# Optimization experiments

Hardware: AMD Instinct MI355X
Metric: run time of the kernel (lower is better)

Reference implementation:

```python
import jax, jax.numpy as jnp
import numpy as np

E, T, H, I, K = 8, 8192, 1024, 4096, 2  # experts, tokens, hidden, intermediate, top_k


def setup_inputs() -> dict:
    key = jax.random.key(0)
    k1, k2, k3, k4 = jax.random.split(key, 4)
    return {
        "hidden_states": jax.random.normal(k1, (T, H), dtype=jnp.float32),
        "router_weight": jax.random.normal(k2, (E, H), dtype=jnp.float32) * 0.02,
        "gate_up_proj": jax.random.normal(k3, (E, 2 * I, H), dtype=jnp.float32) * 0.02,
        "down_proj": jax.random.normal(k4, (E, H, I), dtype=jnp.float32) * 0.02,
    }


def reference(hidden_states, router_weight, gate_up_proj, down_proj):
    x = hidden_states  # [T, H]
    # --- TopKRouter ---
    router_logits = x @ router_weight.T  # [T, E]
    routing_probs = jax.nn.softmax(router_logits.astype(jnp.float32), axis=-1)
    top_k_weights, top_k_indices = jax.lax.top_k(routing_probs, K)  # [T, K]
    top_k_weights = top_k_weights / jnp.sum(top_k_weights, axis=-1, keepdims=True)  # norm_topk_prob
    top_k_weights = top_k_weights.astype(router_logits.dtype)
    # --- MoEExperts: dense combine weight per (token, expert) ---
    # w_dense[t, e] = sum_k top_k_weights[t, k] * (top_k_indices[t, k] == e)
    tok = jnp.arange(x.shape[0])[:, None]
    w_dense = jnp.zeros((x.shape[0], E), dtype=x.dtype).at[tok, top_k_indices].add(top_k_weights)
    out = jnp.zeros_like(x)
    for e in range(E):  # fixed small expert loop (structurally distinct weights)
        gu = x @ gate_up_proj[e].T          # [T, 2I]
        gate, up = jnp.split(gu, 2, axis=-1)
        y = (jax.nn.silu(gate) * up) @ down_proj[e].T  # [T, H]
        out = out + w_dense[:, e:e + 1] * y
    return out
```

## Files before the change

kernel.cpp:

```cpp
#include <hip/hip_runtime.h>
#include <stdint.h>
#include <math.h>

#define NE 8
#define NT 8192
#define NH 1024
#define NI 4096
#define BM 128
#define BK 32

typedef _Float16 half8 __attribute__((ext_vector_type(8)));
typedef float f32x4 __attribute__((ext_vector_type(4)));

#define OFF_X16   (512u << 10)
#define OFF_ACT   (18u << 20)
#define OFF_GUP16 (146ull << 20)
#define OFF_DP16  (274ull << 20)

__device__ __forceinline__ half8 pack_half8(float4 a, float4 b) {
  half8 h;
  h[0] = (_Float16)a.x; h[1] = (_Float16)a.y; h[2] = (_Float16)a.z; h[3] = (_Float16)a.w;
  h[4] = (_Float16)b.x; h[5] = (_Float16)b.y; h[6] = (_Float16)b.z; h[7] = (_Float16)b.w;
  return h;
}

__device__ __forceinline__ void gload16(const void* g, void* l) {
  __builtin_amdgcn_global_load_lds(
      (const __attribute__((address_space(1))) uint32_t*)g,
      (__attribute__((address_space(3))) uint32_t*)l, 16, 0, 0);
}

#define PIPE_WAIT(N) asm volatile("s_waitcnt vmcnt(" #N ")" ::: "memory")
#define PIPE_BAR() do { asm volatile("" ::: "memory"); \
                        __builtin_amdgcn_s_barrier(); \
                        asm volatile("" ::: "memory"); } while (0)

__global__ __launch_bounds__(256) void convert_w(
    const float* __restrict__ src, _Float16* __restrict__ dst, int n8)
{
  int stride = gridDim.x * 256;
  for (int i = blockIdx.x * 256 + threadIdx.x; i < n8; i += stride) {
    const float4* p = (const float4*)(src + (size_t)i * 8);
    float4 a = p[0], b = p[1];
    *(half8*)(dst + (size_t)i * 8) = pack_half8(a, b);
  }
}

__global__ __launch_bounds__(256) void moe_router(
    const float* __restrict__ x, const float* __restrict__ rw,
    int* __restrict__ iws, _Float16* __restrict__ x16)
{
  int wid  = threadIdx.x >> 6;
  int lane = threadIdx.x & 63;
  int t = (blockIdx.x << 2) + wid;

  const float4* xp4 = (const float4*)(x + (size_t)t * NH + lane * 16);
  float xv[16];
  #pragma unroll
  for (int j = 0; j < 4; ++j) {
    float4 v = xp4[j];
    xv[4*j+0] = v.x; xv[4*j+1] = v.y; xv[4*j+2] = v.z; xv[4*j+3] = v.w;
  }
  half8 h0, h1;
  #pragma unroll
  for (int j = 0; j < 8; ++j) { h0[j] = (_Float16)xv[j]; h1[j] = (_Float16)xv[8+j]; }
  half8* xo = (half8*)(x16 + (size_t)t * NH + lane * 16);
  xo[0] = h0; xo[1] = h1;

  float lg[NE];
  #pragma unroll
  for (int e = 0; e < NE; ++e) {
    const float4* wp4 = (const float4*)(rw + e * NH + lane * 16);
    float s = 0.f;
    #pragma unroll
    for (int j = 0; j < 4; ++j) {
      float4 w = wp4[j];
      s += xv[4*j+0]*w.x + xv[4*j+1]*w.y + xv[4*j+2]*w.z + xv[4*j+3]*w.w;
    }
    lg[e] = s;
  }
  #pragma unroll
  for (int d = 32; d > 0; d >>= 1) {
    #pragma unroll
    for (int e = 0; e < NE; ++e) lg[e] += __shfl_xor(lg[e], d, 64);
  }
  if (lane == 0) {
    int e0 = 0;
    #pragma unroll
    for (int e = 1; e < NE; ++e) if (lg[e] > lg[e0]) e0 = e;
    int e1 = (e0 == 0) ? 1 : 0;
    #pragma unroll
    for (int e = 0; e < NE; ++e) if (e != e0 && lg[e] > lg[e1]) e1 = e;
    float p1 = expf(lg[e1] - lg[e0]);
    float s  = 1.f + p1;
    int*   te = iws + 64;
    float* tw = (float*)(iws + 64 + NT*2);
    te[2*t]   = e0; te[2*t+1] = e1;
    tw[2*t]   = 1.f / s; tw[2*t+1] = p1 / s;
    atomicAdd(iws + e0, 1);
    atomicAdd(iws + e1, 1);
  }
}

__global__ void moe_scan(int* iws) {
  if (threadIdx.x == 0 && blockIdx.x == 0) {
    int* cnt = iws; int* off = iws + 8; int* mbc = iws + 25;
    int o = 0, m = 0;
    for (int e = 0; e < NE; ++e) {
      off[e] = o; mbc[e] = m;
      o += cnt[e];
      m += (cnt[e] + BM - 1) / BM;
    }
    off[NE] = o; mbc[NE] = m;
  }
}

__global__ __launch_bounds__(256) void moe_fill(int* __restrict__ iws) {
  int t = blockIdx.x * 256 + threadIdx.x;
  const int*   te = iws + 64;
  const float* tw = (const float*)(iws + 64 + NT*2);
  int*   cursor   = iws + 17;
  const int* off  = iws + 8;
  int*   tok_slot = iws + 64 + NT*4;
  float* w_slot   = (float*)(iws + 64 + NT*6);
  #pragma unroll
  for (int k = 0; k < 2; ++k) {
    int e = te[2*t+k];
    int pos = atomicAdd(&cursor[e], 1);
    int s = off[e] + pos;
    tok_slot[s] = t;
    w_slot[s]   = tw[2*t+k];
  }
}

__global__ __launch_bounds__(256, 2) void moe_gemm1_f16(
    const _Float16* __restrict__ x16, const _Float16* __restrict__ gup16,
    const int* __restrict__ iws, _Float16* __restrict__ act, int i0_base)
{
  const int* cnt = iws; const int* off = iws + 8; const int* mbc = iws + 25;
  const int* tok_slot = iws + 64 + NT*4;
  int bid = blockIdx.x;
  int mb  = bid >> 5;
  int i0  = (i0_base + (bid & 31)) << 6;
  if (mb >= mbc[NE]) return;
  int e = 0;
  while (mb >= mbc[e+1]) ++e;
  int mloc  = mb - mbc[e];
  int row0  = off[e] + mloc * BM;
  int nrows = cnt[e] - mloc * BM; if (nrows > BM) nrows = BM;

  __shared__ __align__(16) _Float16 Al [3][BM * BK];
  __shared__ __align__(16) _Float16 Bgl[3][64 * BK];
  __shared__ __align__(16) _Float16 Bul[3][64 * BK];

  int tid = threadIdx.x, wid = tid >> 6, lane = tid & 63;
  int sr0 = wid*16 + (lane >> 2);
  int sr1 = 64 + sr0;
  int slot = lane & 3;
  int ks0 = (slot ^ ((sr0 >> 1) & 3)) * 8;
  int ks1 = (slot ^ ((sr1 >> 1) & 3)) * 8;

  int tok0 = tok_slot[row0 + (sr0 < nrows ? sr0 : 0)];
  int tok1 = tok_slot[row0 + (sr1 < nrows ? sr1 : 0)];
  const _Float16* pA0 = x16 + (size_t)tok0 * NH + ks0;
  const _Float16* pA1 = x16 + (size_t)tok1 * NH + ks1;
  const _Float16* pBg = gup16 + ((size_t)e*2*NI + i0 + sr0) * NH + ks0;
  const _Float16* pBu = pBg + (size_t)NI * NH;

  int wr = (wid >> 1) * 64, wc = (wid & 1) * 32;
  int fr = lane & 15, fq = lane >> 4;

  f32x4 accG[4][2] = {};
  f32x4 accU[4][2] = {};

  _Float16 *A0 = &Al[0][0], *A1 = &Al[1][0], *A2 = &Al[2][0];
  _Float16 *G0 = &Bgl[0][0], *G1 = &Bgl[1][0], *G2 = &Bgl[2][0];
  _Float16 *U0 = &Bul[0][0], *U1 = &Bul[1][0], *U2 = &Bul[2][0];

#define STAGE1(Ab, Gb, Ub, kk) do { \
    gload16(pA0 + (kk), (Ab) + wid*512); \
    gload16(pA1 + (kk), (Ab) + (4+wid)*512); \
    gload16(pBg + (kk), (Gb) + wid*512); \
    gload16(pBu + (kk), (Ub) + wid*512); \
  } while (0)

#define COMPUTE1(Ab, Gb, Ub) do { \
    half8 aF[4]; \
    _Pragma("unroll") \
    for (int m = 0; m < 4; ++m) { \
      int r = wr + m*16 + fr; \
      aF[m] = *(const half8*)((Ab) + r*BK + ((fq ^ ((r>>1)&3)) * 8)); \
    } \
    __builtin_amdgcn_s_setprio(1); \
    _Pragma("unroll") \
    for (int n = 0; n < 2; ++n) { \
      int rb = wc + n*16 + fr; \
      int bo = rb*BK + ((fq ^ ((rb>>1)&3)) * 8); \
      half8 bg = *(const half8*)((Gb) + bo); \
      half8 bu = *(const half8*)((Ub) + bo); \
      _Pragma("unroll") \
      for (int m = 0; m < 4; ++m) \
        accG[m][n] = __builtin_amdgcn_mfma_f32_16x16x32_f16(aF[m], bg, accG[m][n], 0, 0, 0); \
      _Pragma("unroll") \
      for (int m = 0; m < 4; ++m) \
        accU[m][n] = __builtin_amdgcn_mfma_f32_16x16x32_f16(aF[m], bu, accU[m][n], 0, 0, 0); \
    } \
    __builtin_amdgcn_s_setprio(0); \
  } while (0)

#define ROT1() do { _Float16* t_; \
    t_ = A0; A0 = A1; A1 = A2; A2 = t_; \
    t_ = G0; G0 = G1; G1 = G2; G2 = t_; \
    t_ = U0; U0 = U1; U1 = U2; U2 = t_; } while (0)

  STAGE1(A0, G0, U0, 0);
  STAGE1(A1, G1, U1, BK);

  for (int k0 = 0; k0 + 2*BK < NH; k0 += BK) {
    PIPE_WAIT(4);
    PIPE_BAR();
    STAGE1(A2, G2, U2, k0 + 2*BK);
    COMPUTE1(A0, G0, U0);
    ROT1();
  }
  PIPE_WAIT(4);
  PIPE_BAR();
  COMPUTE1(A0, G0, U0);
  ROT1();
  PIPE_WAIT(0);
  PIPE_BAR();
  COMPUTE1(A0, G0, U0);

#undef STAGE1
#undef COMPUTE1
#undef ROT1

  #pragma unroll
  for (int m = 0; m < 4; ++m) {
    #pragma unroll
    for (int j = 0; j < 4; ++j) {
      int rl = wr + m*16 + fq*4 + j;
      if (rl < nrows) {
        _Float16* dst = act + (size_t)(row0 + rl) * NI + i0 + wc + fr;
        #pragma unroll
        for (int n = 0; n < 2; ++n) {
          float g = accG[m][n][j], u = accU[m][n][j];
          float a = (g / (1.f + __expf(-g))) * u;
          dst[n*16] = (_Float16)a;
        }
      }
    }
  }
}

__global__ __launch_bounds__(256, 2) void moe_gemm2_f16(
    const _Float16* __restrict__ act, const _Float16* __restrict__ dp16,
    const int* __restrict__ iws, float* __restrict__ out)
{
  const int* cnt = iws; const int* off = iws + 8; const int* mbc = iws + 25;
  const int* tok_slot = iws + 64 + NT*4;
  const float* w_slot = (const float*)(iws + 64 + NT*6);
  int bid = blockIdx.x;
  int mb  = ((bid >> 6) << 3) | (bid & 7);
  int h0  = ((bid >> 3) & 7) << 7;
  if (mb >= mbc[NE]) return;
  int e = 0;
  while (mb >= mbc[e+1]) ++e;
  int mloc  = mb - mbc[e];
  int row0  = off[e] + mloc * BM;
  int nrows = cnt[e] - mloc * BM; if (nrows > BM) nrows = BM;

  __shared__ __align__(16) _Float16 Al[3][BM  * BK];
  __shared__ __align__(16) _Float16 Bl[3][128 * BK];

  int tid = threadIdx.x, wid = tid >> 6, lane = tid & 63;
  int sr0 = wid*16 + (lane >> 2);
  int sr1 = 64 + sr0;
  int slot = lane & 3;
  int ks0 = (slot ^ ((sr0 >> 1) & 3)) * 8;
  int ks1 = (slot ^ ((sr1 >> 1) & 3)) * 8;

  const _Float16* pA0 = act + (size_t)(row0 + (sr0 < nrows ? sr0 : 0)) * NI + ks0;
  const _Float16* pA1 = act + (size_t)(row0 + (sr1 < nrows ? sr1 : 0)) * NI + ks1;
  const _Float16* pB0 = dp16 + ((size_t)e*NH + h0 + sr0) * NI + ks0;
  const _Float16* pB1 = dp16 + ((size_t)e*NH + h0 + sr1) * NI + ks1;

  int wr = (wid >> 1) * 64, wc = (wid & 1) * 64;
  int fr = lane & 15, fq = lane >> 4;

  f32x4 acc[4][4] = {};

  _Float16 *A0 = &Al[0][0], *A1 = &Al[1][0], *A2 = &Al[2][0];
  _Float16 *B0 = &Bl[0][0], *B1 = &Bl[1][0], *B2 = &Bl[2][0];

#define STAGE2(Ab, Bb, kk) do { \
    gload16(pA0 + (kk), (Ab) + wid*512); \
    gload16(pA1 + (kk), (Ab) + (4+wid)*512); \
    gload16(pB0 + (kk), (Bb) + wid*512); \
    gload16(pB1 + (kk), (Bb) + (4+wid)*512); \
  } while (0)

#define COMPUTE2(Ab, Bb) do { \
    half8 aF[4]; \
    _Pragma("unroll") \
    for (int m = 0; m < 4; ++m) { \
      int r = wr + m*16 + fr; \
      aF[m] = *(const half8*)((Ab) + r*BK + ((fq ^ ((r>>1)&3)) * 8)); \
    } \
    __builtin_amdgcn_s_setprio(1); \
    _Pragma("unroll") \
    for (int n = 0; n < 4; ++n) { \
      int rb = wc + n*16 + fr; \
      half8 b = *(const half8*)((Bb) + rb*BK + ((fq ^ ((rb>>1)&3)) * 8)); \
      _Pragma("unroll") \
      for (int m = 0; m < 4; ++m) \
        acc[m][n] = __builtin_amdgcn_mfma_f32_16x16x32_f16(aF[m], b, acc[m][n], 0, 0, 0); \
    } \
    __builtin_amdgcn_s_setprio(0); \
  } while (0)

#define ROT2() do { _Float16* t_; \
    t_ = A0; A0 = A1; A1 = A2; A2 = t_; \
    t_ = B0; B0 = B1; B1 = B2; B2 = t_; } while (0)

  STAGE2(A0, B0, 0);
  STAGE2(A1, B1, BK);

  for (int k0 = 0; k0 + 2*BK < NI; k0 += BK) {
    PIPE_WAIT(4);
    PIPE_BAR();
    STAGE2(A2, B2, k0 + 2*BK);
    COMPUTE2(A0, B0);
    ROT2();
  }
  PIPE_WAIT(4);
  PIPE_BAR();
  COMPUTE2(A0, B0);
  ROT2();
  PIPE_WAIT(0);
  PIPE_BAR();
  COMPUTE2(A0, B0);

#undef STAGE2
#undef COMPUTE2
#undef ROT2

  #pragma unroll
  for (int m = 0; m < 4; ++m) {
    #pragma unroll
    for (int j = 0; j < 4; ++j) {
      int rl = wr + m*16 + fq*4 + j;
      if (rl < nrows) {
        int slotr = row0 + rl;
        float wgt = w_slot[slotr];
        int tok   = tok_slot[slotr];
        float* dst = out + (size_t)tok * NH + h0 + wc + fr;
        #pragma unroll
        for (int n = 0; n < 4; ++n)
          atomicAdd(dst + n*16, acc[m][n][j] * wgt);
      }
    }
  }
}

extern "C" void kernel_launch(void* const* d_in, const int* in_sizes, int n_in,
                              void* d_out, int out_size, void* d_ws, size_t ws_size,
                              hipStream_t stream) {
  const float* x   = (const float*)d_in[0];
  const float* rw  = (const float*)d_in[1];
  const float* gup = (const float*)d_in[2];
  const float* dp  = (const float*)d_in[3];
  float* out = (float*)d_out;
  int* iws = (int*)d_ws;
  _Float16* x16   = (_Float16*)((char*)d_ws + OFF_X16);
  _Float16* act   = (_Float16*)((char*)d_ws + OFF_ACT);
  _Float16* gup16 = (_Float16*)((char*)d_ws + OFF_GUP16);
  _Float16* dp16  = (_Float16*)((char*)d_ws + OFF_DP16);

  hipMemsetAsync(d_out, 0, (size_t)NT * NH * sizeof(float), stream);
  hipMemsetAsync(d_ws, 0, 512, stream);

  convert_w<<<4096, 256, 0, stream>>>(gup, gup16, NE*2*NI*NH/8);
  convert_w<<<4096, 256, 0, stream>>>(dp,  dp16,  NE*NH*NI/8);

  moe_router<<<NT / 4, 256, 0, stream>>>(x, rw, iws, x16);
  moe_scan<<<1, 64, 0, stream>>>(iws);
  moe_fill<<<NT / 256, 256, 0, stream>>>(iws);

  int nmb = NT * 2 / BM + NE;
  moe_gemm1_f16<<<nmb * 32, 256, 0, stream>>>(x16, gup16, iws, act, 0);
  moe_gemm1_f16<<<nmb * 32, 256, 0, stream>>>(x16, gup16, iws, act, 32);
  moe_gemm2_f16<<<nmb * (NH / 128), 256, 0, stream>>>(act, dp16, iws, out);
}
```

Measured before the change: 982.5 us.

## Fuse fp32-to-fp16 weight conversion into GEMM tile loads

Drops the standalone weight conversion kernels and has both expert GEMMs load fp32 weight tiles directly into LDS, converting to fp16 when building MFMA fragments. This removes a full read-write pass over all expert weights before the GEMMs. In exchange, each GEMM tile fetches twice as many weight bytes, repeated across m-blocks. LDS use per block also grows, and per-fragment conversion instructions are added to the inner loop.

```diff
diff --git a/kernel.cpp b/kernel.cpp
--- a/kernel.cpp
+++ b/kernel.cpp
@@ -14,15 +14,6 @@
 
 #define OFF_X16   (512u << 10)
 #define OFF_ACT   (18u << 20)
-#define OFF_GUP16 (146ull << 20)
-#define OFF_DP16  (274ull << 20)
-
-__device__ __forceinline__ half8 pack_half8(float4 a, float4 b) {
-  half8 h;
-  h[0] = (_Float16)a.x; h[1] = (_Float16)a.y; h[2] = (_Float16)a.z; h[3] = (_Float16)a.w;
-  h[4] = (_Float16)b.x; h[5] = (_Float16)b.y; h[6] = (_Float16)b.z; h[7] = (_Float16)b.w;
-  return h;
-}
 
 __device__ __forceinline__ void gload16(const void* g, void* l) {
   __builtin_amdgcn_global_load_lds(
@@ -34,17 +25,6 @@
 #define PIPE_BAR() do { asm volatile("" ::: "memory"); \
                         __builtin_amdgcn_s_barrier(); \
                         asm volatile("" ::: "memory"); } while (0)
-
-__global__ __launch_bounds__(256) void convert_w(
-    const float* __restrict__ src, _Float16* __restrict__ dst, int n8)
-{
-  int stride = gridDim.x * 256;
-  for (int i = blockIdx.x * 256 + threadIdx.x; i < n8; i += stride) {
-    const float4* p = (const float4*)(src + (size_t)i * 8);
-    float4 a = p[0], b = p[1];
-    *(half8*)(dst + (size_t)i * 8) = pack_half8(a, b);
-  }
-}
 
 __global__ __launch_bounds__(256) void moe_router(
     const float* __restrict__ x, const float* __restrict__ rw,
@@ -133,8 +113,20 @@
   }
 }
 
+
+#define LDBF(Bp, r) __extension__({ \
+    const float* _b = (Bp) + (size_t)(r) * 32; \
+    f32x4 _lo = *(const f32x4*)(_b + ((((fq<<1)  ) ^ ((r)&7)) << 2)); \
+    f32x4 _hi = *(const f32x4*)(_b + ((((fq<<1)|1) ^ ((r)&7)) << 2)); \
+    half8 _h; \
+    _h[0]=(_Float16)_lo[0]; _h[1]=(_Float16)_lo[1]; \
+    _h[2]=(_Float16)_lo[2]; _h[3]=(_Float16)_lo[3]; \
+    _h[4]=(_Float16)_hi[0]; _h[5]=(_Float16)_hi[1]; \
+    _h[6]=(_Float16)_hi[2]; _h[7]=(_Float16)_hi[3]; \
+    _h; })
+
 __global__ __launch_bounds__(256, 2) void moe_gemm1_f16(
-    const _Float16* __restrict__ x16, const _Float16* __restrict__ gup16,
+    const _Float16* __restrict__ x16, const float* __restrict__ gup,
     const int* __restrict__ iws, _Float16* __restrict__ act, int i0_base)
 {
   const int* cnt = iws; const int* off = iws + 8; const int* mbc = iws + 25;
@@ -150,22 +142,25 @@
   int nrows = cnt[e] - mloc * BM; if (nrows > BM) nrows = BM;
 
   __shared__ __align__(16) _Float16 Al [3][BM * BK];
-  __shared__ __align__(16) _Float16 Bgl[3][64 * BK];
-  __shared__ __align__(16) _Float16 Bul[3][64 * BK];
+  __shared__ __align__(16) float    Bgl[3][64 * BK];
+  __shared__ __align__(16) float    Bul[3][64 * BK];
 
   int tid = threadIdx.x, wid = tid >> 6, lane = tid & 63;
   int sr0 = wid*16 + (lane >> 2);
   int sr1 = 64 + sr0;
-  int slot = lane & 3;
-  int ks0 = (slot ^ ((sr0 >> 1) & 3)) * 8;
-  int ks1 = (slot ^ ((sr1 >> 1) & 3)) * 8;
-
+  int slotA = lane & 3;
+  int ksA0 = (slotA ^ ((sr0 >> 1) & 3)) * 8;
+  int ksA1 = (slotA ^ ((sr1 >> 1) & 3)) * 8;
   int tok0 = tok_slot[row0 + (sr0 < nrows ? sr0 : 0)];
   int tok1 = tok_slot[row0 + (sr1 < nrows ? sr1 : 0)];
-  const _Float16* pA0 = x16 + (size_t)tok0 * NH + ks0;
-  const _Float16* pA1 = x16 + (size_t)tok1 * NH + ks1;
-  const _Float16* pBg = gup16 + ((size_t)e*2*NI + i0 + sr0) * NH + ks0;
-  const _Float16* pBu = pBg + (size_t)NI * NH;
+  const _Float16* pA0 = x16 + (size_t)tok0 * NH + ksA0;
+  const _Float16* pA1 = x16 + (size_t)tok1 * NH + ksA1;
+
+  int srB   = tid >> 3;
+  int slotB = tid & 7;
+  int ksB   = ((slotB ^ (srB & 7)) << 2);
+  const float* pBg = gup + ((size_t)e*2*NI + i0 + srB) * NH + ksB;
+  const float* pBu = pBg + (size_t)NI * NH;
 
   int wr = (wid >> 1) * 64, wc = (wid & 1) * 32;
   int fr = lane & 15, fq = lane >> 4;
@@ -174,14 +169,16 @@
   f32x4 accU[4][2] = {};
 
   _Float16 *A0 = &Al[0][0], *A1 = &Al[1][0], *A2 = &Al[2][0];
-  _Float16 *G0 = &Bgl[0][0], *G1 = &Bgl[1][0], *G2 = &Bgl[2][0];
-  _Float16 *U0 = &Bul[0][0], *U1 = &Bul[1][0], *U2 = &Bul[2][0];
+  float *G0 = &Bgl[0][0], *G1 = &Bgl[1][0], *G2 = &Bgl[2][0];
+  float *U0 = &Bul[0][0], *U1 = &Bul[1][0], *U2 = &Bul[2][0];
 
 #define STAGE1(Ab, Gb, Ub, kk) do { \
     gload16(pA0 + (kk), (Ab) + wid*512); \
     gload16(pA1 + (kk), (Ab) + (4+wid)*512); \
-    gload16(pBg + (kk), (Gb) + wid*512); \
-    gload16(pBu + (kk), (Ub) + wid*512); \
+    gload16(pBg + (kk),             (Gb) + wid*256); \
+    gload16(pBg + 32*(size_t)NH + (kk), (Gb) + 1024 + wid*256); \
+    gload16(pBu + (kk),             (Ub) + wid*256); \
+    gload16(pBu + 32*(size_t)NH + (kk), (Ub) + 1024 + wid*256); \
   } while (0)
 
 #define COMPUTE1(Ab, Gb, Ub) do { \
@@ -195,9 +192,8 @@
     _Pragma("unroll") \
     for (int n = 0; n < 2; ++n) { \
       int rb = wc + n*16 + fr; \
-      int bo = rb*BK + ((fq ^ ((rb>>1)&3)) * 8); \
-      half8 bg = *(const half8*)((Gb) + bo); \
-      half8 bu = *(const half8*)((Ub) + bo); \
+      half8 bg = LDBF((Gb), rb); \
+      half8 bu = LDBF((Ub), rb); \
       _Pragma("unroll") \
       for (int m = 0; m < 4; ++m) \
         accG[m][n] = __builtin_amdgcn_mfma_f32_16x16x32_f16(aF[m], bg, accG[m][n], 0, 0, 0); \
@@ -208,22 +204,22 @@
     __builtin_amdgcn_s_setprio(0); \
   } while (0)
 
-#define ROT1() do { _Float16* t_; \
-    t_ = A0; A0 = A1; A1 = A2; A2 = t_; \
-    t_ = G0; G0 = G1; G1 = G2; G2 = t_; \
-    t_ = U0; U0 = U1; U1 = U2; U2 = t_; } while (0)
+#define ROT1() do { _Float16* ta_; float* tb_; \
+    ta_ = A0; A0 = A1; A1 = A2; A2 = ta_; \
+    tb_ = G0; G0 = G1; G1 = G2; G2 = tb_; \
+    tb_ = U0; U0 = U1; U1 = U2; U2 = tb_; } while (0)
 
   STAGE1(A0, G0, U0, 0);
   STAGE1(A1, G1, U1, BK);
 
   for (int k0 = 0; k0 + 2*BK < NH; k0 += BK) {
-    PIPE_WAIT(4);
+    PIPE_WAIT(6);
     PIPE_BAR();
     STAGE1(A2, G2, U2, k0 + 2*BK);
     COMPUTE1(A0, G0, U0);
     ROT1();
   }
-  PIPE_WAIT(4);
+  PIPE_WAIT(6);
   PIPE_BAR();
   COMPUTE1(A0, G0, U0);
   ROT1();
@@ -254,7 +250,7 @@
 }
 
 __global__ __launch_bounds__(256, 2) void moe_gemm2_f16(
-    const _Float16* __restrict__ act, const _Float16* __restrict__ dp16,
+    const _Float16* __restrict__ act, const float* __restrict__ dp,
     const int* __restrict__ iws, float* __restrict__ out)
 {
   const int* cnt = iws; const int* off = iws + 8; const int* mbc = iws + 25;
@@ -271,19 +267,21 @@
   int nrows = cnt[e] - mloc * BM; if (nrows > BM) nrows = BM;
 
   __shared__ __align__(16) _Float16 Al[3][BM  * BK];
-  __shared__ __align__(16) _Float16 Bl[3][128 * BK];
+  __shared__ __align__(16) float    Bl[3][128 * BK];
 
   int tid = threadIdx.x, wid = tid >> 6, lane = tid & 63;
   int sr0 = wid*16 + (lane >> 2);
   int sr1 = 64 + sr0;
-  int slot = lane & 3;
-  int ks0 = (slot ^ ((sr0 >> 1) & 3)) * 8;
-  int ks1 = (slot ^ ((sr1 >> 1) & 3)) * 8;
-
-  const _Float16* pA0 = act + (size_t)(row0 + (sr0 < nrows ? sr0 : 0)) * NI + ks0;
-  const _Float16* pA1 = act + (size_t)(row0 + (sr1 < nrows ? sr1 : 0)) * NI + ks1;
-  const _Float16* pB0 = dp16 + ((size_t)e*NH + h0 + sr0) * NI + ks0;
-  const _Float16* pB1 = dp16 + ((size_t)e*NH + h0 + sr1) * NI + ks1;
+  int slotA = lane & 3;
+  int ksA0 = (slotA ^ ((sr0 >> 1) & 3)) * 8;
+  int ksA1 = (slotA ^ ((sr1 >> 1) & 3)) * 8;
+  const _Float16* pA0 = act + (size_t)(row0 + (sr0 < nrows ? sr0 : 0)) * NI + ksA0;
+  const _Float16* pA1 = act + (size_t)(row0 + (sr1 < nrows ? sr1 : 0)) * NI + ksA1;
+
+  int srB   = tid >> 3;
+  int slotB = tid & 7;
+  int ksB   = ((slotB ^ (srB & 7)) << 2);
+  const float* pB = dp + ((size_t)e*NH + h0 + srB) * NI + ksB;
 
   int wr = (wid >> 1) * 64, wc = (wid & 1) * 64;
   int fr = lane & 15, fq = lane >> 4;
@@ -291,13 +289,15 @@
   f32x4 acc[4][4] = {};
 
   _Float16 *A0 = &Al[0][0], *A1 = &Al[1][0], *A2 = &Al[2][0];
-  _Float16 *B0 = &Bl[0][0], *B1 = &Bl[1][0], *B2 = &Bl[2][0];
+  float *B0 = &Bl[0][0], *B1 = &Bl[1][0], *B2 = &Bl[2][0];
 
 #define STAGE2(Ab, Bb, kk) do { \
     gload16(pA0 + (kk), (Ab) + wid*512); \
     gload16(pA1 + (kk), (Ab) + (4+wid)*512); \
-    gload16(pB0 + (kk), (Bb) + wid*512); \
-    gload16(pB1 + (kk), (Bb) + (4+wid)*512); \
+    gload16(pB + (kk),                  (Bb) + wid*256); \
+    gload16(pB + 32*(size_t)NI + (kk),  (Bb) + 1024 + wid*256); \
+    gload16(pB + 64*(size_t)NI + (kk),  (Bb) + 2048 + wid*256); \
+    gload16(pB + 96*(size_t)NI + (kk),  (Bb) + 3072 + wid*256); \
   } while (0)
 
 #define COMPUTE2(Ab, Bb) do { \
@@ -311,7 +311,7 @@
     _Pragma("unroll") \
     for (int n = 0; n < 4; ++n) { \
       int rb = wc + n*16 + fr; \
-      half8 b = *(const half8*)((Bb) + rb*BK + ((fq ^ ((rb>>1)&3)) * 8)); \
+      half8 b = LDBF((Bb), rb); \
       _Pragma("unroll") \
       for (int m = 0; m < 4; ++m) \
         acc[m][n] = __builtin_amdgcn_mfma_f32_16x16x32_f16(aF[m], b, acc[m][n], 0, 0, 0); \
@@ -319,21 +319,21 @@
     __builtin_amdgcn_s_setprio(0); \
   } while (0)
 
-#define ROT2() do { _Float16* t_; \
-    t_ = A0; A0 = A1; A1 = A2; A2 = t_; \
-    t_ = B0; B0 = B1; B1 = B2; B2 = t_; } while (0)
+#define ROT2() do { _Float16* ta_; float* tb_; \
+    ta_ = A0; A0 = A1; A1 = A2; A2 = ta_; \
+    tb_ = B0; B0 = B1; B1 = B2; B2 = tb_; } while (0)
 
   STAGE2(A0, B0, 0);
   STAGE2(A1, B1, BK);
 
   for (int k0 = 0; k0 + 2*BK < NI; k0 += BK) {
-    PIPE_WAIT(4);
+    PIPE_WAIT(6);
     PIPE_BAR();
     STAGE2(A2, B2, k0 + 2*BK);
     COMPUTE2(A0, B0);
     ROT2();
   }
-  PIPE_WAIT(4);
+  PIPE_WAIT(6);
   PIPE_BAR();
   COMPUTE2(A0, B0);
   ROT2();
@@ -372,23 +372,18 @@
   const float* dp  = (const float*)d_in[3];
   float* out = (float*)d_out;
   int* iws = (int*)d_ws;
-  _Float16* x16   = (_Float16*)((char*)d_ws + OFF_X16);
-  _Float16* act   = (_Float16*)((char*)d_ws + OFF_ACT);
-  _Float16* gup16 = (_Float16*)((char*)d_ws + OFF_GUP16);
-  _Float16* dp16  = (_Float16*)((char*)d_ws + OFF_DP16);
+  _Float16* x16 = (_Float16*)((char*)d_ws + OFF_X16);
+  _Float16* act = (_Float16*)((char*)d_ws + OFF_ACT);
 
   hipMemsetAsync(d_out, 0, (size_t)NT * NH * sizeof(float), stream);
   hipMemsetAsync(d_ws, 0, 512, stream);
-
-  convert_w<<<4096, 256, 0, stream>>>(gup, gup16, NE*2*NI*NH/8);
-  convert_w<<<4096, 256, 0, stream>>>(dp,  dp16,  NE*NH*NI/8);
 
   moe_router<<<NT / 4, 256, 0, stream>>>(x, rw, iws, x16);
   moe_scan<<<1, 64, 0, stream>>>(iws);
   moe_fill<<<NT / 256, 256, 0, stream>>>(iws);
 
   int nmb = NT * 2 / BM + NE;
-  moe_gemm1_f16<<<nmb * 32, 256, 0, stream>>>(x16, gup16, iws, act, 0);
-  moe_gemm1_f16<<<nmb * 32, 256, 0, stream>>>(x16, gup16, iws, act, 32);
-  moe_gemm2_f16<<<nmb * (NH / 128), 256, 0, stream>>>(act, dp16, iws, out);
-}
+  moe_gemm1_f16<<<nmb * 32, 256, 0, stream>>>(x16, gup, iws, act, 0);
+  moe_gemm1_f16<<<nmb * 32, 256, 0, stream>>>(x16, gup, iws, act, 32);
+  moe_gemm2_f16<<<nmb * (NH / 128), 256, 0, stream>>>(act, dp, iws, out);
+}
```

Result: slower. 1.365 ms (+38.9%).
